# Optimization experiments

Hardware: AMD Instinct MI355X
Metric: run time of the kernel (lower is better)

The kernel has to match this reference:

```python
import jax, jax.numpy as jnp
import numpy as np

QUERY_DIM = 512
INNER_DIM = 2 * QUERY_DIM  # 1024
CROSS_DIM = 512


def setup_inputs() -> dict:
    key = jax.random.key(0)
    k1, k2, k3, k4, k5, k6, k7 = jax.random.split(key, 7)
    B, N1, N2 = 8, 2048, 2048
    S1 = jax.random.normal(k1, (B, N1, CROSS_DIM), dtype=jnp.float32)
    S2 = jax.random.normal(k2, (B, N2, QUERY_DIM), dtype=jnp.float32)
    # Linear weights stored as [in, out] (pre-transposed vs torch's [out, in])
    sq = 1.0 / np.sqrt(QUERY_DIM)
    sc = 1.0 / np.sqrt(CROSS_DIM)
    si = 1.0 / np.sqrt(INNER_DIM)
    Wq = jax.random.uniform(k3, (QUERY_DIM, INNER_DIM), jnp.float32, -sq, sq)
    Wk = jax.random.uniform(k4, (CROSS_DIM, INNER_DIM), jnp.float32, -sc, sc)
    Wv = jax.random.uniform(k5, (CROSS_DIM, INNER_DIM), jnp.float32, -sc, sc)
    Wo = jax.random.uniform(k6, (INNER_DIM, QUERY_DIM), jnp.float32, -si, si)
    bo = jax.random.uniform(k7, (QUERY_DIM,), jnp.float32, -si, si)
    return {"S1": S1, "S2": S2, "Wq": Wq, "Wk": Wk, "Wv": Wv, "Wo": Wo, "bo": bo}


def reference(S1, S2, Wq, Wk, Wv, Wo, bo):
    # softmax((Wq S2)(Wk S1)^T) (Wv S1), then output projection. NOTE: no 1/sqrt(d) scaling.
    query = jnp.einsum('bnd,de->bne', S2, Wq)   # [B, N2, inner]
    key_ = jnp.einsum('bmd,de->bme', S1, Wk)    # [B, N1, inner]
    value = jnp.einsum('bmd,de->bme', S1, Wv)   # [B, N1, inner]
    scores = jnp.einsum('bne,bme->bnm', query, key_)  # [B, N2, N1]
    attn = jax.nn.softmax(scores, axis=-1)
    masked = jnp.einsum('bnm,bme->bne', attn, value)  # [B, N2, inner]
    out = jnp.einsum('bne,ed->bnd', masked, Wo) + bo  # [B, N2, query_dim]
    return out
```

## Files before the change

### kernel.cpp

```cpp
#include <hip/hip_runtime.h>


typedef _Float16 h_t;
typedef _Float16 h8 __attribute__((ext_vector_type(8)));
typedef _Float16 h4 __attribute__((ext_vector_type(4)));
typedef float f4 __attribute__((ext_vector_type(4)));

#define MFMA16(a, b, c) __builtin_amdgcn_mfma_f32_16x16x32_f16(a, b, c, 0, 0, 0)

typedef const __attribute__((address_space(1))) void* gas_t;
typedef __attribute__((address_space(3))) void* las_t;

__device__ __forceinline__ void gl2lds16(const void* g, void* l) {
    __builtin_amdgcn_global_load_lds((gas_t)g, (las_t)l, 16, 0, 0);
}

__global__ __launch_bounds__(256) void k_cast5(const float* __restrict__ S1,
                                               const float* __restrict__ S2,
                                               const float* __restrict__ Wq,
                                               const float* __restrict__ Wk,
                                               const float* __restrict__ Wv,
                                               h_t* __restrict__ S1h,
                                               h_t* __restrict__ S2h,
                                               h_t* __restrict__ Wqh,
                                               h_t* __restrict__ Wkh,
                                               h_t* __restrict__ Wvh) {
    long i = (long)blockIdx.x * 256 + threadIdx.x;
    const long n = 2097152;
    const long wn = 131072;
    const float* src;
    h_t* dst;
    long off;
    if (i < n) { src = S1; dst = S1h; off = i; }
    else if (i < 2 * n) { src = S2; dst = S2h; off = i - n; }
    else if (i < 2 * n + wn) { src = Wq; dst = Wqh; off = i - 2 * n; }
    else if (i < 2 * n + 2 * wn) { src = Wk; dst = Wkh; off = i - 2 * n - wn; }
    else { src = Wv; dst = Wvh; off = i - 2 * n - 2 * wn; }
    float4 v = *((const float4*)src + off);
    h4 h = {(h_t)v.x, (h_t)v.y, (h_t)v.z, (h_t)v.w};
    *((h4*)dst + off) = h;
}

__global__ __launch_bounds__(256) void k_transpose_o(const float* __restrict__ Wo,
                                                     h_t* __restrict__ Wot) {
    const int K = 1024, N = 512;
    int kb = blockIdx.y * 32, nb = blockIdx.x * 32;
    __shared__ float tile[32][33];
    int x = threadIdx.x & 31, y = threadIdx.x >> 5;
#pragma unroll
    for (int j = 0; j < 4; j++)
        tile[y + j * 8][x] = Wo[(size_t)(kb + y + j * 8) * N + nb + x];
    __syncthreads();
#pragma unroll
    for (int j = 0; j < 4; j++)
        Wot[(size_t)(nb + y + j * 8) * K + kb + x] = (h_t)tile[x][y + j * 8];
}

__global__ __launch_bounds__(256) void k_wpre(const h_t* __restrict__ Wqh,
                                              const h_t* __restrict__ Wkh,
                                              const h_t* __restrict__ Wot,
                                              const h_t* __restrict__ Wvh,
                                              h_t* __restrict__ Wkq,
                                              h_t* __restrict__ Wvot) {
    __shared__ h_t As[128 * 64];
    __shared__ h_t Bs[128 * 64];
    int t = threadIdx.x, w = t >> 6, lane = t & 63;
    int q16 = lane >> 4, l16 = lane & 15;
    int id = blockIdx.x;
    const h_t* A;
    const h_t* Bt;
    h_t* C;
    if (id < 16) { A = Wkh; Bt = Wqh; C = Wkq; }
    else { id -= 16; A = Wot; Bt = Wvh; C = Wvot; }
    size_t m0 = (size_t)(id >> 2) * 128, n0 = (size_t)(id & 3) * 128;
    const int K = 1024, N = 512;
    int wr = (w >> 1) * 64, wc = (w & 1) * 64;
    f4 acc[4][4] = {};

    for (int k0 = 0; k0 < K; k0 += 64) {
#pragma unroll
        for (int j = 0; j < 4; j++) {
            int q = w * 4 + j;
            int row = q * 8 + (lane >> 3);
            int ks = (((lane & 7) ^ (row & 7)) << 3);
            gl2lds16(A + (m0 + row) * K + k0 + ks, &As[q * 512]);
            gl2lds16(Bt + (n0 + row) * K + k0 + ks, &Bs[q * 512]);
        }
        __syncthreads();
#pragma unroll
        for (int ks = 0; ks < 2; ks++) {
            h8 av[4], bv[4];
#pragma unroll
            for (int i = 0; i < 4; i++) {
                int row = wr + i * 16 + l16;
                int ch = ks * 4 + q16;
                av[i] = *(const h8*)&As[row * 64 + ((ch ^ (row & 7)) << 3)];
            }
#pragma unroll
            for (int j = 0; j < 4; j++) {
                int row = wc + j * 16 + l16;
                int ch = ks * 4 + q16;
                bv[j] = *(const h8*)&Bs[row * 64 + ((ch ^ (row & 7)) << 3)];
            }
#pragma unroll
            for (int i = 0; i < 4; i++)
#pragma unroll
                for (int j = 0; j < 4; j++)
                    acc[i][j] = MFMA16(av[i], bv[j], acc[i][j]);
        }
        __syncthreads();
    }
#pragma unroll
    for (int i = 0; i < 4; i++) {
        size_t r0 = m0 + wr + i * 16 + q16 * 4;
#pragma unroll
        for (int j = 0; j < 4; j++) {
            size_t c = n0 + wc + j * 16 + l16;
#pragma unroll
            for (int r = 0; r < 4; r++)
                C[(r0 + r) * N + c] = (h_t)acc[i][j][r];
        }
    }
}

__global__ __launch_bounds__(256) void k_proj2(const h_t* __restrict__ S2h,
                                               const h_t* __restrict__ S1h,
                                               const h_t* __restrict__ Wkq,
                                               const h_t* __restrict__ Wvot,
                                               const float* __restrict__ bo,
                                               h_t* __restrict__ T,
                                               h_t* __restrict__ Vt) {
    __shared__ h_t As[128 * 64];
    __shared__ h_t Bs[128 * 64];
    int t = threadIdx.x, w = t >> 6, lane = t & 63;
    int q16 = lane >> 4, l16 = lane & 15;
    int id = blockIdx.x;
    int mode = id >> 9;
    id &= 511;
    const h_t* A = mode ? S1h : S2h;
    const h_t* Bt = mode ? Wvot : Wkq;
    size_t m0 = (size_t)(id >> 2) * 128, n0 = (size_t)(id & 3) * 128;
    const int K = 512, N = 512;
    int wr = (w >> 1) * 64, wc = (w & 1) * 64;
    f4 acc[4][4] = {};

    for (int k0 = 0; k0 < K; k0 += 64) {
#pragma unroll
        for (int j = 0; j < 4; j++) {
            int q = w * 4 + j;
            int row = q * 8 + (lane >> 3);
            int ks = (((lane & 7) ^ (row & 7)) << 3);
            gl2lds16(A + (m0 + row) * K + k0 + ks, &As[q * 512]);
            gl2lds16(Bt + (n0 + row) * K + k0 + ks, &Bs[q * 512]);
        }
        __syncthreads();
#pragma unroll
        for (int ks = 0; ks < 2; ks++) {
            h8 av[4], bv[4];
#pragma unroll
            for (int i = 0; i < 4; i++) {
                int row = wr + i * 16 + l16;
                int ch = ks * 4 + q16;
                av[i] = *(const h8*)&As[row * 64 + ((ch ^ (row & 7)) << 3)];
            }
#pragma unroll
            for (int j = 0; j < 4; j++) {
                int row = wc + j * 16 + l16;
                int ch = ks * 4 + q16;
                bv[j] = *(const h8*)&Bs[row * 64 + ((ch ^ (row & 7)) << 3)];
            }
#pragma unroll
            for (int i = 0; i < 4; i++)
#pragma unroll
                for (int j = 0; j < 4; j++)
                    acc[i][j] = MFMA16(av[i], bv[j], acc[i][j]);
        }
        __syncthreads();
    }
    if (mode == 0) {
#pragma unroll
        for (int i = 0; i < 4; i++) {
            size_t r0 = m0 + wr + i * 16 + q16 * 4;
#pragma unroll
            for (int j = 0; j < 4; j++) {
                size_t c = n0 + wc + j * 16 + l16;
#pragma unroll
                for (int r = 0; r < 4; r++)
                    T[(r0 + r) * 512 + c] = (h_t)acc[i][j][r];
            }
        }
    } else {
#pragma unroll
        for (int i = 0; i < 4; i++) {
            size_t gm = m0 + wr + i * 16 + q16 * 4;
            size_t b = gm >> 11;
            size_t n = gm & 2047;
#pragma unroll
            for (int j = 0; j < 4; j++) {
                size_t d = n0 + wc + j * 16 + l16;
                float bias = bo[d];
                h4 hv = {(h_t)(acc[i][j][0] + bias), (h_t)(acc[i][j][1] + bias),
                         (h_t)(acc[i][j][2] + bias), (h_t)(acc[i][j][3] + bias)};
                *(h4*)&Vt[(b * 512 + d) * 2048 + n] = hv;
            }
        }
    }
}

__global__ __launch_bounds__(256) void k_qk(const h_t* __restrict__ T,
                                            const h_t* __restrict__ S1h,
                                            h_t* __restrict__ P,
                                            float2* __restrict__ Mkt,
                                            int qh) {
    __shared__ h_t sm[16384];
    __shared__ float pmx[2][128], psm[2][128];
    h_t* As = sm;
    h_t* Bs = sm + 8192;
    int t = threadIdx.x, w = t >> 6, lane = t & 63;
    int q16 = lane >> 4, l16 = lane & 15;
    int qt = blockIdx.x, kt = blockIdx.y, b = blockIdx.z;
    const h_t* A = T + ((size_t)b * 2048 + qh * 1024 + qt * 128) * 512;
    const h_t* Bt = S1h + ((size_t)b * 2048 + kt * 128) * 512;
    int wr = (w >> 1) * 64, wc = (w & 1) * 64;
    f4 acc[4][4] = {};

    for (int k0 = 0; k0 < 512; k0 += 64) {
#pragma unroll
        for (int j = 0; j < 4; j++) {
            int q = w * 4 + j;
            int row = q * 8 + (lane >> 3);
            int ks = (((lane & 7) ^ (row & 7)) << 3);
            gl2lds16(A + (size_t)row * 512 + k0 + ks, &As[q * 512]);
            gl2lds16(Bt + (size_t)row * 512 + k0 + ks, &Bs[q * 512]);
        }
        __syncthreads();
#pragma unroll
        for (int ks = 0; ks < 2; ks++) {
            h8 av[4], bv[4];
#pragma unroll
            for (int i = 0; i < 4; i++) {
                int row = wr + i * 16 + l16;
                int ch = ks * 4 + q16;
                av[i] = *(const h8*)&As[row * 64 + ((ch ^ (row & 7)) << 3)];
            }
#pragma unroll
            for (int j = 0; j < 4; j++) {
                int row = wc + j * 16 + l16;
                int ch = ks * 4 + q16;
                bv[j] = *(const h8*)&Bs[row * 64 + ((ch ^ (row & 7)) << 3)];
            }
#pragma unroll
            for (int i = 0; i < 4; i++)
#pragma unroll
                for (int j = 0; j < 4; j++)
                    acc[i][j] = MFMA16(av[i], bv[j], acc[i][j]);
        }
        __syncthreads();
    }
    float lm[4][4], ls[4][4];
#pragma unroll
    for (int i = 0; i < 4; i++)
#pragma unroll
        for (int r = 0; r < 4; r++) {
            float m = acc[i][0][r];
#pragma unroll
            for (int j = 1; j < 4; j++) m = fmaxf(m, acc[i][j][r]);
            lm[i][r] = m;
        }
#pragma unroll
    for (int msk = 1; msk <= 8; msk <<= 1)
#pragma unroll
        for (int i = 0; i < 4; i++)
#pragma unroll
            for (int r = 0; r < 4; r++)
                lm[i][r] = fmaxf(lm[i][r], __shfl_xor(lm[i][r], msk, 64));
#pragma unroll
    for (int i = 0; i < 4; i++)
#pragma unroll
        for (int r = 0; r < 4; r++) {
            float s = 0.f;
#pragma unroll
            for (int j = 0; j < 4; j++) s += __expf(acc[i][j][r] - lm[i][r]);
            ls[i][r] = s;
        }
#pragma unroll
    for (int msk = 1; msk <= 8; msk <<= 1)
#pragma unroll
        for (int i = 0; i < 4; i++)
#pragma unroll
            for (int r = 0; r < 4; r++)
                ls[i][r] += __shfl_xor(ls[i][r], msk, 64);
    if (l16 == 0) {
#pragma unroll
        for (int i = 0; i < 4; i++)
#pragma unroll
            for (int r = 0; r < 4; r++) {
                pmx[w & 1][wr + i * 16 + q16 * 4 + r] = lm[i][r];
                psm[w & 1][wr + i * 16 + q16 * 4 + r] = ls[i][r];
            }
    }
    __syncthreads();
#pragma unroll
    for (int i = 0; i < 4; i++)
#pragma unroll
        for (int r = 0; r < 4; r++) {
            int row = wr + i * 16 + q16 * 4 + r;
            float om = pmx[(w & 1) ^ 1][row];
            float os = psm[(w & 1) ^ 1][row];
            float M = fmaxf(lm[i][r], om);
            float L = ls[i][r] * __expf(lm[i][r] - M) + os * __expf(om - M);
            lm[i][r] = M;
            ls[i][r] = L;
        }
    if ((w & 1) == 0 && l16 == 0) {
#pragma unroll
        for (int i = 0; i < 4; i++)
#pragma unroll
            for (int r = 0; r < 4; r++)
                Mkt[((size_t)b * 16 + kt) * 1024 + qt * 128 + wr + i * 16 + q16 * 4 + r] =
                    make_float2(lm[i][r], ls[i][r]);
    }
#pragma unroll
    for (int i = 0; i < 4; i++)
#pragma unroll
        for (int j = 0; j < 4; j++)
#pragma unroll
            for (int r = 0; r < 4; r++)
                sm[(wr + i * 16 + q16 * 4 + r) * 128 + wc + j * 16 + l16] =
                    (h_t)__expf(acc[i][j][r] - lm[i][r]);
    __syncthreads();
    size_t Pbase = ((size_t)b * 1024 + qt * 128) * 2048 + (size_t)kt * 128;
#pragma unroll
    for (int p = 0; p < 8; p++) {
        int row = p * 16 + (t >> 4);
        int c8 = (t & 15) * 8;
        *(h8*)(P + Pbase + (size_t)row * 2048 + c8) = *(const h8*)&sm[row * 128 + c8];
    }
}

__global__ __launch_bounds__(256) void k_stats(const float2* __restrict__ Mkt,
                                               float2* __restrict__ MF) {
    int r = blockIdx.x * 256 + threadIdx.x;
    int b = r >> 10, rowl = r & 1023;
    float2 v[16];
    float m = -1e30f;
#pragma unroll
    for (int kt = 0; kt < 16; kt++) {
        v[kt] = Mkt[((size_t)b * 16 + kt) * 1024 + rowl];
        m = fmaxf(m, v[kt].x);
    }
    float l = 0.f;
#pragma unroll
    for (int kt = 0; kt < 16; kt++) l += v[kt].y * __expf(v[kt].x - m);
    MF[(size_t)b * 1024 + rowl] = make_float2(m, 1.f / l);
}

__global__ __launch_bounds__(256) void k_pv(const h_t* __restrict__ P,
                                            const h_t* __restrict__ Vt,
                                            const float2* __restrict__ Mkt,
                                            const float2* __restrict__ MF,
                                            float* __restrict__ Out,
                                            int qh) {
    __shared__ h_t As[64 * 64];
    __shared__ h_t Bs[128 * 64];
    int t = threadIdx.x, w = t >> 6, lane = t & 63;
    int q16 = lane >> 4, l16 = lane & 15;
    int rt = blockIdx.x, dt = blockIdx.y, b = blockIdx.z;
    int rg = w >> 1, dg = w & 1;
    int sr = t >> 3, sc = t & 7;
    float mf0 = MF[(size_t)b * 1024 + rt * 64 + sr].x;
    float mf1 = MF[(size_t)b * 1024 + rt * 64 + 32 + sr].x;
    const h_t* Pb = P + ((size_t)b * 1024 + rt * 64) * 2048;
    const h_t* Vb = Vt + ((size_t)b * 512 + dt * 128) * 2048;
    f4 acc[2][4] = {};

    for (int k0 = 0; k0 < 2048; k0 += 64) {
        int kt = k0 >> 7;
#pragma unroll
        for (int p = 0; p < 2; p++) {
            int r_ = p * 32 + sr;
            float mfin = p ? mf1 : mf0;
            float2 mk = Mkt[((size_t)b * 16 + kt) * 1024 + rt * 64 + r_];
            float dl = __expf(mk.x - mfin);
            h_t dh = (h_t)dl;
            h8 dv = {dh, dh, dh, dh, dh, dh, dh, dh};
            h8 v = *(const h8*)(Pb + (size_t)r_ * 2048 + k0 + sc * 8);
            v = v * dv;
            *(h8*)&As[r_ * 64 + ((sc ^ (r_ & 7)) << 3)] = v;
        }
#pragma unroll
        for (int j = 0; j < 4; j++) {
            int q = w * 4 + j;
            int row = q * 8 + (lane >> 3);
            int ks = (((lane & 7) ^ (row & 7)) << 3);
            gl2lds16(Vb + (size_t)row * 2048 + k0 + ks, &Bs[q * 512]);
        }
        __syncthreads();
#pragma unroll
        for (int ks = 0; ks < 2; ks++) {
            int ch = ks * 4 + q16;
            h8 av[2], bv[4];
#pragma unroll
            for (int i = 0; i < 2; i++) {
                int row = rg * 32 + i * 16 + l16;
                av[i] = *(const h8*)&As[row * 64 + ((ch ^ (row & 7)) << 3)];
            }
#pragma unroll
            for (int j = 0; j < 4; j++) {
                int dr = dg * 64 + j * 16 + l16;
                bv[j] = *(const h8*)&Bs[dr * 64 + ((ch ^ (dr & 7)) << 3)];
            }
#pragma unroll
            for (int i = 0; i < 2; i++)
#pragma unroll
                for (int j = 0; j < 4; j++)
                    acc[i][j] = MFMA16(av[i], bv[j], acc[i][j]);
        }
        __syncthreads();
    }
#pragma unroll
    for (int i = 0; i < 2; i++)
#pragma unroll
        for (int rr = 0; rr < 4; rr++) {
            int row = rg * 32 + i * 16 + q16 * 4 + rr;
            float linv = MF[(size_t)b * 1024 + rt * 64 + row].y;
#pragma unroll
            for (int j = 0; j < 4; j++) {
                int d = dt * 128 + dg * 64 + j * 16 + l16;
                Out[((size_t)b * 2048 + qh * 1024 + rt * 64 + row) * 512 + d] =
                    acc[i][j][rr] * linv;
            }
        }
}

extern "C" void kernel_launch(void* const* d_in, const int* in_sizes, int n_in,
                              void* d_out, int out_size, void* d_ws, size_t ws_size,
                              hipStream_t stream) {
    const float* S1 = (const float*)d_in[0];
    const float* S2 = (const float*)d_in[1];
    const float* Wq = (const float*)d_in[2];
    const float* Wk = (const float*)d_in[3];
    const float* Wv = (const float*)d_in[4];
    const float* Wo = (const float*)d_in[5];
    const float* bo = (const float*)d_in[6];
    float* Out = (float*)d_out;

    char* ws = (char*)d_ws;
    h_t* S2h  = (h_t*)(ws);
    h_t* S1h  = (h_t*)(ws + 16777216);
    h_t* Wqh  = (h_t*)(ws + 33554432);
    h_t* Wkh  = (h_t*)(ws + 34603008);
    h_t* Wvh  = (h_t*)(ws + 35651584);
    h_t* Wot  = (h_t*)(ws + 36700160);
    h_t* Wkq  = (h_t*)(ws + 37748736);
    h_t* Wvot = (h_t*)(ws + 38273024);
    h_t* T    = (h_t*)(ws + 38797312);
    h_t* Vt   = (h_t*)(ws + 55574528);
    h_t* Phb  = (h_t*)(ws + 72351744);
    float2* Mkt = (float2*)(ws + 105906176);
    float2* MF  = (float2*)(ws + 106954752);

    k_cast5<<<17920, 256, 0, stream>>>(S1, S2, Wq, Wk, Wv, S1h, S2h, Wqh, Wkh, Wvh);
    k_transpose_o<<<dim3(16, 32), 256, 0, stream>>>(Wo, Wot);
    k_wpre<<<32, 256, 0, stream>>>(Wqh, Wkh, Wot, Wvh, Wkq, Wvot);
    k_proj2<<<1024, 256, 0, stream>>>(S2h, S1h, Wkq, Wvot, bo, T, Vt);
    for (int qh = 0; qh < 2; qh++) {
        k_qk<<<dim3(8, 16, 8), 256, 0, stream>>>(T, S1h, Phb, Mkt, qh);
        k_stats<<<32, 256, 0, stream>>>(Mkt, MF);
        k_pv<<<dim3(16, 4, 8), 256, 0, stream>>>(Phb, Vt, Mkt, MF, Out, qh);
    }
}
```

Measured before the change: 326.4 us.

## Fuse query halves into single launches and use exp2 with precomputed rescale factors

Removes the two-pass loop over query halves so k_qk, k_stats and k_pv each run once over all 2048 query rows, using larger grids and a reorganized workspace that aliases buffers. It folds log2(e) into the Wkq weight product so softmax can use exp2f, and reuses the computed exponentials instead of recomputing them. k_stats now emits per-tile fp16 rescale factors, so k_pv loads one factor per 128-column tile instead of computing an exp per 64-column step. The cost is a larger P buffer and aliasing S1h with Dkt and S2h with P, which relies on launch ordering being correct.

```diff
diff --git a/kernel.cpp b/kernel.cpp
--- a/kernel.cpp
+++ b/kernel.cpp
@@ -70,8 +70,9 @@
     const h_t* A;
     const h_t* Bt;
     h_t* C;
-    if (id < 16) { A = Wkh; Bt = Wqh; C = Wkq; }
-    else { id -= 16; A = Wot; Bt = Wvh; C = Wvot; }
+    float oscale;
+    if (id < 16) { A = Wkh; Bt = Wqh; C = Wkq; oscale = 1.44269504f; }
+    else { id -= 16; A = Wot; Bt = Wvh; C = Wvot; oscale = 1.0f; }
     size_t m0 = (size_t)(id >> 2) * 128, n0 = (size_t)(id & 3) * 128;
     const int K = 1024, N = 512;
     int wr = (w >> 1) * 64, wc = (w & 1) * 64;
@@ -118,7 +119,7 @@
             size_t c = n0 + wc + j * 16 + l16;
 #pragma unroll
             for (int r = 0; r < 4; r++)
-                C[(r0 + r) * N + c] = (h_t)acc[i][j][r];
+                C[(r0 + r) * N + c] = (h_t)(acc[i][j][r] * oscale);
         }
     }
 }
@@ -140,7 +141,7 @@
     const h_t* A = mode ? S1h : S2h;
     const h_t* Bt = mode ? Wvot : Wkq;
     size_t m0 = (size_t)(id >> 2) * 128, n0 = (size_t)(id & 3) * 128;
-    const int K = 512, N = 512;
+    const int K = 512;
     int wr = (w >> 1) * 64, wc = (w & 1) * 64;
     f4 acc[4][4] = {};
 
@@ -210,8 +211,7 @@
 __global__ __launch_bounds__(256) void k_qk(const h_t* __restrict__ T,
                                             const h_t* __restrict__ S1h,
                                             h_t* __restrict__ P,
-                                            float2* __restrict__ Mkt,
-                                            int qh) {
+                                            float2* __restrict__ Mkt) {
     __shared__ h_t sm[16384];
     __shared__ float pmx[2][128], psm[2][128];
     h_t* As = sm;
@@ -219,7 +219,7 @@
     int t = threadIdx.x, w = t >> 6, lane = t & 63;
     int q16 = lane >> 4, l16 = lane & 15;
     int qt = blockIdx.x, kt = blockIdx.y, b = blockIdx.z;
-    const h_t* A = T + ((size_t)b * 2048 + qh * 1024 + qt * 128) * 512;
+    const h_t* A = T + ((size_t)b * 2048 + qt * 128) * 512;
     const h_t* Bt = S1h + ((size_t)b * 2048 + kt * 128) * 512;
     int wr = (w >> 1) * 64, wc = (w & 1) * 64;
     f4 acc[4][4] = {};
@@ -280,7 +280,11 @@
         for (int r = 0; r < 4; r++) {
             float s = 0.f;
 #pragma unroll
-            for (int j = 0; j < 4; j++) s += __expf(acc[i][j][r] - lm[i][r]);
+            for (int j = 0; j < 4; j++) {
+                float e = exp2f(acc[i][j][r] - lm[i][r]);
+                acc[i][j][r] = e;
+                s += e;
+            }
             ls[i][r] = s;
         }
 #pragma unroll
@@ -308,18 +312,12 @@
             float om = pmx[(w & 1) ^ 1][row];
             float os = psm[(w & 1) ^ 1][row];
             float M = fmaxf(lm[i][r], om);
-            float L = ls[i][r] * __expf(lm[i][r] - M) + os * __expf(om - M);
-            lm[i][r] = M;
-            ls[i][r] = L;
-        }
-    if ((w & 1) == 0 && l16 == 0) {
-#pragma unroll
-        for (int i = 0; i < 4; i++)
-#pragma unroll
-            for (int r = 0; r < 4; r++)
-                Mkt[((size_t)b * 16 + kt) * 1024 + qt * 128 + wr + i * 16 + q16 * 4 + r] =
-                    make_float2(lm[i][r], ls[i][r]);
-    }
+            float sc = exp2f(lm[i][r] - M);
+            float L = ls[i][r] * sc + os * exp2f(om - M);
+            if ((w & 1) == 0 && l16 == 0)
+                Mkt[((size_t)b * 16 + kt) * 2048 + qt * 128 + row] = make_float2(M, L);
+            lm[i][r] = sc;
+        }
 #pragma unroll
     for (int i = 0; i < 4; i++)
 #pragma unroll
@@ -327,9 +325,9 @@
 #pragma unroll
             for (int r = 0; r < 4; r++)
                 sm[(wr + i * 16 + q16 * 4 + r) * 128 + wc + j * 16 + l16] =
-                    (h_t)__expf(acc[i][j][r] - lm[i][r]);
+                    (h_t)(acc[i][j][r] * lm[i][r]);
     __syncthreads();
-    size_t Pbase = ((size_t)b * 1024 + qt * 128) * 2048 + (size_t)kt * 128;
+    size_t Pbase = ((size_t)b * 2048 + qt * 128) * 2048 + (size_t)kt * 128;
 #pragma unroll
     for (int p = 0; p < 8; p++) {
         int row = p * 16 + (t >> 4);
@@ -339,28 +337,32 @@
 }
 
 __global__ __launch_bounds__(256) void k_stats(const float2* __restrict__ Mkt,
-                                               float2* __restrict__ MF) {
+                                               float2* __restrict__ MF,
+                                               h_t* __restrict__ Dkt) {
     int r = blockIdx.x * 256 + threadIdx.x;
-    int b = r >> 10, rowl = r & 1023;
+    int b = r >> 11, rowl = r & 2047;
     float2 v[16];
     float m = -1e30f;
 #pragma unroll
     for (int kt = 0; kt < 16; kt++) {
-        v[kt] = Mkt[((size_t)b * 16 + kt) * 1024 + rowl];
+        v[kt] = Mkt[((size_t)b * 16 + kt) * 2048 + rowl];
         m = fmaxf(m, v[kt].x);
     }
     float l = 0.f;
 #pragma unroll
-    for (int kt = 0; kt < 16; kt++) l += v[kt].y * __expf(v[kt].x - m);
-    MF[(size_t)b * 1024 + rowl] = make_float2(m, 1.f / l);
+    for (int kt = 0; kt < 16; kt++) {
+        float d = exp2f(v[kt].x - m);
+        l += v[kt].y * d;
+        Dkt[((size_t)b * 16 + kt) * 2048 + rowl] = (h_t)d;
+    }
+    MF[(size_t)b * 2048 + rowl] = make_float2(m, 1.f / l);
 }
 
 __global__ __launch_bounds__(256) void k_pv(const h_t* __restrict__ P,
                                             const h_t* __restrict__ Vt,
-                                            const float2* __restrict__ Mkt,
+                                            const h_t* __restrict__ Dkt,
                                             const float2* __restrict__ MF,
-                                            float* __restrict__ Out,
-                                            int qh) {
+                                            float* __restrict__ Out) {
     __shared__ h_t As[64 * 64];
     __shared__ h_t Bs[128 * 64];
     int t = threadIdx.x, w = t >> 6, lane = t & 63;
@@ -368,66 +370,66 @@
     int rt = blockIdx.x, dt = blockIdx.y, b = blockIdx.z;
     int rg = w >> 1, dg = w & 1;
     int sr = t >> 3, sc = t & 7;
-    float mf0 = MF[(size_t)b * 1024 + rt * 64 + sr].x;
-    float mf1 = MF[(size_t)b * 1024 + rt * 64 + 32 + sr].x;
-    const h_t* Pb = P + ((size_t)b * 1024 + rt * 64) * 2048;
+    const h_t* Pb = P + ((size_t)b * 2048 + rt * 64) * 2048;
     const h_t* Vb = Vt + ((size_t)b * 512 + dt * 128) * 2048;
     f4 acc[2][4] = {};
 
-    for (int k0 = 0; k0 < 2048; k0 += 64) {
-        int kt = k0 >> 7;
-#pragma unroll
-        for (int p = 0; p < 2; p++) {
-            int r_ = p * 32 + sr;
-            float mfin = p ? mf1 : mf0;
-            float2 mk = Mkt[((size_t)b * 16 + kt) * 1024 + rt * 64 + r_];
-            float dl = __expf(mk.x - mfin);
-            h_t dh = (h_t)dl;
-            h8 dv = {dh, dh, dh, dh, dh, dh, dh, dh};
-            h8 v = *(const h8*)(Pb + (size_t)r_ * 2048 + k0 + sc * 8);
-            v = v * dv;
-            *(h8*)&As[r_ * 64 + ((sc ^ (r_ & 7)) << 3)] = v;
-        }
-#pragma unroll
-        for (int j = 0; j < 4; j++) {
-            int q = w * 4 + j;
-            int row = q * 8 + (lane >> 3);
-            int ks = (((lane & 7) ^ (row & 7)) << 3);
-            gl2lds16(Vb + (size_t)row * 2048 + k0 + ks, &Bs[q * 512]);
-        }
-        __syncthreads();
-#pragma unroll
-        for (int ks = 0; ks < 2; ks++) {
-            int ch = ks * 4 + q16;
-            h8 av[2], bv[4];
-#pragma unroll
-            for (int i = 0; i < 2; i++) {
-                int row = rg * 32 + i * 16 + l16;
-                av[i] = *(const h8*)&As[row * 64 + ((ch ^ (row & 7)) << 3)];
-            }
-#pragma unroll
-            for (int j = 0; j < 4; j++) {
-                int dr = dg * 64 + j * 16 + l16;
-                bv[j] = *(const h8*)&Bs[dr * 64 + ((ch ^ (dr & 7)) << 3)];
-            }
-#pragma unroll
-            for (int i = 0; i < 2; i++)
-#pragma unroll
-                for (int j = 0; j < 4; j++)
-                    acc[i][j] = MFMA16(av[i], bv[j], acc[i][j]);
-        }
-        __syncthreads();
+    for (int kt = 0; kt < 16; kt++) {
+        h_t d0 = Dkt[((size_t)b * 16 + kt) * 2048 + rt * 64 + sr];
+        h_t d1 = Dkt[((size_t)b * 16 + kt) * 2048 + rt * 64 + 32 + sr];
+#pragma unroll
+        for (int h = 0; h < 2; h++) {
+            int k0 = kt * 128 + h * 64;
+#pragma unroll
+            for (int p = 0; p < 2; p++) {
+                int r_ = p * 32 + sr;
+                h_t dh = p ? d1 : d0;
+                h8 dv = {dh, dh, dh, dh, dh, dh, dh, dh};
+                h8 v = *(const h8*)(Pb + (size_t)r_ * 2048 + k0 + sc * 8);
+                v = v * dv;
+                *(h8*)&As[r_ * 64 + ((sc ^ (r_ & 7)) << 3)] = v;
+            }
+#pragma unroll
+            for (int j = 0; j < 4; j++) {
+                int q = w * 4 + j;
+                int row = q * 8 + (lane >> 3);
+                int ks = (((lane & 7) ^ (row & 7)) << 3);
+                gl2lds16(Vb + (size_t)row * 2048 + k0 + ks, &Bs[q * 512]);
+            }
+            __syncthreads();
+#pragma unroll
+            for (int ks = 0; ks < 2; ks++) {
+                int ch = ks * 4 + q16;
+                h8 av[2], bv[4];
+#pragma unroll
+                for (int i = 0; i < 2; i++) {
+                    int row = rg * 32 + i * 16 + l16;
+                    av[i] = *(const h8*)&As[row * 64 + ((ch ^ (row & 7)) << 3)];
+                }
+#pragma unroll
+                for (int j = 0; j < 4; j++) {
+                    int dr = dg * 64 + j * 16 + l16;
+                    bv[j] = *(const h8*)&Bs[dr * 64 + ((ch ^ (dr & 7)) << 3)];
+                }
+#pragma unroll
+                for (int i = 0; i < 2; i++)
+#pragma unroll
+                    for (int j = 0; j < 4; j++)
+                        acc[i][j] = MFMA16(av[i], bv[j], acc[i][j]);
+            }
+            __syncthreads();
+        }
     }
 #pragma unroll
     for (int i = 0; i < 2; i++)
 #pragma unroll
         for (int rr = 0; rr < 4; rr++) {
             int row = rg * 32 + i * 16 + q16 * 4 + rr;
-            float linv = MF[(size_t)b * 1024 + rt * 64 + row].y;
+            float linv = MF[(size_t)b * 2048 + rt * 64 + row].y;
 #pragma unroll
             for (int j = 0; j < 4; j++) {
                 int d = dt * 128 + dg * 64 + j * 16 + l16;
-                Out[((size_t)b * 2048 + qh * 1024 + rt * 64 + row) * 512 + d] =
+                Out[((size_t)b * 2048 + rt * 64 + row) * 512 + d] =
                     acc[i][j][rr] * linv;
             }
         }
@@ -446,27 +448,26 @@
     float* Out = (float*)d_out;
 
     char* ws = (char*)d_ws;
-    h_t* S2h  = (h_t*)(ws);
-    h_t* S1h  = (h_t*)(ws + 16777216);
-    h_t* Wqh  = (h_t*)(ws + 33554432);
-    h_t* Wkh  = (h_t*)(ws + 34603008);
-    h_t* Wvh  = (h_t*)(ws + 35651584);
-    h_t* Wot  = (h_t*)(ws + 36700160);
-    h_t* Wkq  = (h_t*)(ws + 37748736);
-    h_t* Wvot = (h_t*)(ws + 38273024);
-    h_t* T    = (h_t*)(ws + 38797312);
-    h_t* Vt   = (h_t*)(ws + 55574528);
-    h_t* Phb  = (h_t*)(ws + 72351744);
-    float2* Mkt = (float2*)(ws + 105906176);
-    float2* MF  = (float2*)(ws + 106954752);
+    h_t* S1h  = (h_t*)(ws);
+    h_t* T    = (h_t*)(ws + 16777216);
+    h_t* Vt   = (h_t*)(ws + 33554432);
+    h_t* P    = (h_t*)(ws + 50331648);
+    float2* Mkt = (float2*)(ws + 117440512);
+    h_t* S2h  = (h_t*)(ws + 50331648);
+    h_t* Wqh  = (h_t*)(ws + 67108864);
+    h_t* Wkh  = (h_t*)(ws + 68157440);
+    h_t* Wvh  = (h_t*)(ws + 69206016);
+    h_t* Wot  = (h_t*)(ws + 70254592);
+    h_t* Wkq  = (h_t*)(ws + 71303168);
+    h_t* Wvot = (h_t*)(ws + 71827456);
+    h_t* Dkt  = (h_t*)(ws);
+    float2* MF = (float2*)(ws + 524288);
 
     k_cast5<<<17920, 256, 0, stream>>>(S1, S2, Wq, Wk, Wv, S1h, S2h, Wqh, Wkh, Wvh);
     k_transpose_o<<<dim3(16, 32), 256, 0, stream>>>(Wo, Wot);
     k_wpre<<<32, 256, 0, stream>>>(Wqh, Wkh, Wot, Wvh, Wkq, Wvot);
     k_proj2<<<1024, 256, 0, stream>>>(S2h, S1h, Wkq, Wvot, bo, T, Vt);
-    for (int qh = 0; qh < 2; qh++) {
-        k_qk<<<dim3(8, 16, 8), 256, 0, stream>>>(T, S1h, Phb, Mkt, qh);
-        k_stats<<<32, 256, 0, stream>>>(Mkt, MF);
-        k_pv<<<dim3(16, 4, 8), 256, 0, stream>>>(Phb, Vt, Mkt, MF, Out, qh);
-    }
-}
+    k_qk<<<dim3(16, 16, 8), 256, 0, stream>>>(T, S1h, P, Mkt);
+    k_stats<<<64, 256, 0, stream>>>(Mkt, MF, Dkt);
+    k_pv<<<dim3(32, 4, 8), 256, 0, stream>>>(P, Vt, Dkt, MF, Out);
+}
```

Result: faster. 293.2 us (-10.2%).
